# Kernel tuning notes

Hardware: AMD Instinct MI355X
Metric: run time of the kernel (lower is better)

Reference implementation:

```python
import jax, jax.numpy as jnp
import numpy as np

N = 100000   # nodes
F = 256      # input features
H = 128      # hidden_dim
E = 3200000  # edges
EPS = 1e-5   # LayerNorm eps (torch default)


def setup_inputs() -> dict:
    key = jax.random.key(0)
    ks = jax.random.split(key, 8)
    x = jax.random.normal(ks[0], (N, F), dtype=jnp.float32)
    edge_index = jax.random.randint(ks[1], (2, E), 0, N, dtype=jnp.int64)
    W1 = jax.random.normal(ks[2], (F, H), dtype=jnp.float32) * 0.05
    b1 = jnp.zeros((H,), jnp.float32)
    g1 = jnp.ones((H,), jnp.float32)
    be1 = jnp.zeros((H,), jnp.float32)
    W2 = jax.random.normal(ks[3], (H, H // 2), dtype=jnp.float32) * 0.05
    b2 = jnp.zeros((H // 2,), jnp.float32)
    g2 = jnp.ones((H // 2,), jnp.float32)
    be2 = jnp.zeros((H // 2,), jnp.float32)
    Wr = jax.random.normal(ks[4], (H // 2, 1), dtype=jnp.float32) * 0.05
    br = jnp.zeros((1,), jnp.float32)
    return {"x": x, "edge_index": edge_index, "W1": W1, "b1": b1, "g1": g1,
            "be1": be1, "W2": W2, "b2": b2, "g2": g2, "be2": be2,
            "Wr": Wr, "br": br}


def gcn_conv(x, src, dst, norm, W, b, n):
    # transform then propagate: out[dst] += norm_e * (x @ W)[src]
    h = x @ W                                   # [n, out]
    msg = h[src] * norm[:, None]                # [E+n, out] gather + scale
    out = jax.ops.segment_sum(msg, dst, num_segments=n)  # scatter-add
    return out + b


def layer_norm(x, g, b):
    mu = jnp.mean(x, axis=-1, keepdims=True)
    var = jnp.mean(jnp.square(x - mu), axis=-1, keepdims=True)
    return (x - mu) * jax.lax.rsqrt(var + EPS) * g + b


def reference(x, edge_index, W1, b1, g1, be1, W2, b2, g2, be2, Wr, br):
    n = x.shape[0]
    loop = jnp.arange(n, dtype=edge_index.dtype)
    src = jnp.concatenate([edge_index[0], loop])  # self-loops appended
    dst = jnp.concatenate([edge_index[1], loop])
    # symmetric normalization: deg includes self-loop, so deg >= 1
    deg = jax.ops.segment_sum(jnp.ones_like(src, dtype=x.dtype), dst, num_segments=n)
    dinv = jax.lax.rsqrt(deg)
    norm = dinv[src] * dinv[dst]                # [E+n]

    h = gcn_conv(x, src, dst, norm, W1, b1, n)
    h = jax.nn.relu(layer_norm(h, g1, be1))     # dropout is identity in eval
    h = gcn_conv(h, src, dst, norm, W2, b2, n)
    h = jax.nn.relu(layer_norm(h, g2, be2))
    out = jax.nn.sigmoid(h @ Wr + br)           # [N, 1]
    # torch .squeeze(0) is a no-op since N != 1
    return out
```

## Files before the change

### kernel.cpp

```cpp
#include <hip/hip_runtime.h>
#include <math.h>
#include <stdint.h>


#define DEG_CAP 96
#define MAXBUCKET 400
#define BSHIFT 8
#define SCAN_B 1024

typedef _Float16 half_t;
typedef __attribute__((ext_vector_type(2))) _Float16 half2v;
typedef __attribute__((ext_vector_type(8))) _Float16 half8;
typedef __attribute__((ext_vector_type(4))) float f32x4;
typedef __attribute__((ext_vector_type(2))) float f32x2;

__device__ __forceinline__ uint32_t pack2(float a, float b) {
    half2v h; h.x = (half_t)a; h.y = (half_t)b;
    return __builtin_bit_cast(uint32_t, h);
}
__device__ __forceinline__ float2 unpack2(uint32_t u) {
    half2v h = __builtin_bit_cast(half2v, u);
    return make_float2((float)h.x, (float)h.y);
}

__device__ __forceinline__ float wave_reduce_sum(float x) {
#pragma unroll
    for (int o = 32; o >= 1; o >>= 1) x += __shfl_xor(x, o, 64);
    return x;
}

__global__ void k_detect(const int* __restrict__ ei, int* __restrict__ flag,
                         uint32_t* __restrict__ h1s, uint32_t* __restrict__ h2s,
                         int N) {
    const int t = threadIdx.x;
    if (t == 0) {
        int all_zero = 1;
        for (int i = 1; i < 128; i += 2)
            if (ei[i] != 0) all_zero = 0;
        *flag = all_zero;
    }
    if (t < 32) h1s[(size_t)N * 32 + t] = 0;
    else if (t < 48) h2s[(size_t)N * 16 + (t - 32)] = 0;
}

__device__ __forceinline__ int load_idx(const int* __restrict__ ei,
                                        long long pos, int is64) {
    if (is64) return (int)((const long long*)ei)[pos];
    return ei[pos];
}

__global__ __launch_bounds__(256) void k_w1t(const float* __restrict__ W1,
                                             uint16_t* __restrict__ w1t) {
    int idx = blockIdx.x * 256 + threadIdx.x;
    int m = idx >> 8, k = idx & 255;
    half_t v = (half_t)W1[k * 128 + m];
    w1t[idx] = __builtin_bit_cast(uint16_t, v);
}

__global__ __launch_bounds__(256) void k_hist(
    const int* __restrict__ ei, const int* __restrict__ flag,
    int* __restrict__ blkcnt, long long E, int P, int nbucket, int chunk) {
    __shared__ int hist[MAXBUCKET];
    for (int j = threadIdx.x; j < nbucket; j += 256) hist[j] = 0;
    __syncthreads();
    const int is64 = *flag;
    long long c0 = (long long)blockIdx.x * chunk;
    long long c1 = c0 + chunk; if (c1 > E) c1 = E;
    for (long long e = c0 + threadIdx.x; e < c1; e += 256) {
        int d = load_idx(ei, E + e, is64);
        atomicAdd(&hist[d >> BSHIFT], 1);
    }
    __syncthreads();
    for (int j = threadIdx.x; j < nbucket; j += 256)
        blkcnt[j * P + blockIdx.x] = hist[j];
}

__global__ __launch_bounds__(SCAN_B) void k_scan_local(
    const int* __restrict__ in, int* __restrict__ pre,
    int* __restrict__ partials, int M) {
    __shared__ int sh[SCAN_B];
    int i = blockIdx.x * SCAN_B + threadIdx.x;
    int v = (i < M) ? in[i] : 0;
    sh[threadIdx.x] = v;
    __syncthreads();
    for (int o = 1; o < SCAN_B; o <<= 1) {
        int t = (threadIdx.x >= o) ? sh[threadIdx.x - o] : 0;
        __syncthreads();
        sh[threadIdx.x] += t;
        __syncthreads();
    }
    if (i < M) pre[i] = sh[threadIdx.x] - v;
    if (threadIdx.x == SCAN_B - 1) partials[blockIdx.x] = sh[SCAN_B - 1];
}

__global__ __launch_bounds__(1024) void k_scan_partials(
    const int* __restrict__ partials, int* __restrict__ pscan, int NB) {
    __shared__ int sh[1024];
    int v = (threadIdx.x < NB) ? partials[threadIdx.x] : 0;
    sh[threadIdx.x] = v;
    __syncthreads();
    for (int o = 1; o < 1024; o <<= 1) {
        int t = (threadIdx.x >= o) ? sh[threadIdx.x - o] : 0;
        __syncthreads();
        sh[threadIdx.x] += t;
        __syncthreads();
    }
    pscan[threadIdx.x] = sh[threadIdx.x] - v;
}

__global__ __launch_bounds__(SCAN_B) void k_scan_add(
    const int* __restrict__ pre, const int* __restrict__ pscan,
    int* __restrict__ boff, int M) {
    int i = blockIdx.x * SCAN_B + threadIdx.x;
    if (i < M) boff[i] = pre[i] + pscan[blockIdx.x];
}

__global__ __launch_bounds__(256) void k_scatter_gemm(
    const int* __restrict__ ei, const int* __restrict__ flag,
    const int* __restrict__ boff, int2* __restrict__ ebuf,
    const float* __restrict__ x, const uint16_t* __restrict__ w1t,
    uint32_t* __restrict__ h1w, int n_gemm, int P, int nbucket, int chunk,
    long long E, int N) {
    __shared__ uint32_t xhw[64 * 132];
    __shared__ int cur[MAXBUCKET];
    const int sub = blockIdx.x % 3, grp = blockIdx.x / 3;

    if (sub == 0) {
        if (grp >= P) return;
        const int is64 = *flag;
        for (int j = threadIdx.x; j < nbucket; j += 256)
            cur[j] = boff[j * P + grp];
        __syncthreads();
        long long c0 = (long long)grp * chunk;
        long long c1 = c0 + chunk; if (c1 > E) c1 = E;
        for (long long e = c0 + threadIdx.x; e < c1; e += 256) {
            int s = load_idx(ei, e, is64);
            int d = load_idx(ei, E + e, is64);
            int pos = atomicAdd(&cur[d >> BSHIFT], 1);
            ebuf[pos] = make_int2(s, d & ((1 << BSHIFT) - 1));
        }
        return;
    }

    const int gb = grp * 2 + (sub - 1);
    if (gb >= n_gemm) return;
    const int t = threadIdx.x;
    const int row0 = gb * 64;

#pragma unroll
    for (int i = 0; i < 16; ++i) {
        int idx = t + i * 256;
        int r = idx >> 6, c4 = idx & 63;
        int rg = row0 + r; if (rg >= N) rg = N - 1;
        float4 v = ((const float4*)(x + (long long)rg * 256))[c4];
        uint2 p;
        p.x = pack2(v.x, v.y);
        p.y = pack2(v.z, v.w);
        *(uint2*)&xhw[r * 132 + 2 * c4] = p;
    }
    __syncthreads();

    const int lane = t & 63, w = t >> 6;
    const int r = lane & 15, g = lane >> 4;
    const int node = row0 + 16 * w + r;

    f32x4 acc[8];
#pragma unroll
    for (int mt = 0; mt < 8; ++mt) acc[mt] = (f32x4)0.0f;

    const uint32_t* xrow = &xhw[(16 * w + r) * 132];
#pragma unroll
    for (int ks = 0; ks < 8; ++ks) {
        half8 bfr = *(const half8*)&xrow[16 * ks + 4 * g];
#pragma unroll
        for (int mt = 0; mt < 8; ++mt) {
            half8 afr = *(const half8*)(w1t + ((16 * mt + r) * 256 + 32 * ks + 8 * g));
            acc[mt] = __builtin_amdgcn_mfma_f32_16x16x32_f16(afr, bfr, acc[mt], 0, 0, 0);
        }
    }

    if (node < N) {
#pragma unroll
        for (int mt = 0; mt < 8; ++mt) {
            uint2 pv;
            pv.x = pack2(acc[mt][0], acc[mt][1]);
            pv.y = pack2(acc[mt][2], acc[mt][3]);
            *(uint2*)&h1w[(long long)node * 64 + 8 * mt + 2 * g] = pv;
        }
    }
}

__global__ __launch_bounds__(256) void k_rankplace(
    const int2* __restrict__ ebuf, const int* __restrict__ boff,
    int* __restrict__ csr, int* __restrict__ cnt, float* __restrict__ dinv,
    const uint32_t* __restrict__ h1, uint16_t* __restrict__ h1s,
    int P, int nbucket, int N, long long E) {
    __shared__ int c256[256];
    __shared__ float dl[256];
    const int k = blockIdx.x;
    c256[threadIdx.x] = 0;
    __syncthreads();
    const int beg = boff[k * P];
    const int end = (k + 1 < nbucket) ? boff[(k + 1) * P] : (int)E;
    for (int i = beg + threadIdx.x; i < end; i += 256) {
        int2 sd = ebuf[i];
        int r = atomicAdd(&c256[sd.y], 1);
        if (r < DEG_CAP) csr[((k << BSHIFT) + sd.y) * DEG_CAP + r] = sd.x;
    }
    __syncthreads();
    const int base_node = k << BSHIFT;
    const int node = base_node + threadIdx.x;
    float dv = rsqrtf((float)c256[threadIdx.x] + 1.0f);
    dl[threadIdx.x] = dv;
    if (node < N) {
        cnt[node] = c256[threadIdx.x];
        dinv[node] = dv;
        int cn = min(c256[threadIdx.x], DEG_CAP);
        int cnp = (cn + 15) & ~15;
        for (int r = cn; r < cnp; ++r) csr[node * DEG_CAP + r] = N;
    }
    __syncthreads();
    const int nloc = min(256, N - base_node);
    for (int i = threadIdx.x; i < nloc * 64; i += 256) {
        const int loc = i >> 6;
        const float dvl = dl[loc];
        const long long w = (long long)(base_node + loc) * 64 + (i & 63);
        float2 v = unpack2(h1[w]);
        int p = __builtin_amdgcn_cvt_pk_fp8_f32(v.x * dvl, v.y * dvl, 0, false);
        h1s[w] = (uint16_t)p;
    }
}

__global__ __launch_bounds__(512) void k_agg1(
    const int* __restrict__ cnt, const float* __restrict__ dinv,
    const int* __restrict__ csr, const uint8_t* __restrict__ h1s,
    const float* __restrict__ b, const float* __restrict__ g,
    const float* __restrict__ be, const float* __restrict__ W2,
    uint8_t* __restrict__ h2s, int N) {
    __shared__ float W2s[128 * 64];
    __shared__ float zs[8][132];
    const int t = threadIdx.x;

#pragma unroll
    for (int i = 0; i < 4; ++i) {
        int idx = t + i * 512;
        ((float4*)W2s)[idx] = ((const float4*)W2)[idx];
    }
    __syncthreads();

    const int lane = t & 63, wave = t >> 6;
    const int node = blockIdx.x * 8 + wave;
    if (node >= N) return;

    const float di = dinv[node];
    const int cn = min(cnt[node], DEG_CAP);
    const int cnp = (cn + 15) & ~15;
    const int base = node * DEG_CAP;
    const int loff = lane << 1;

    uint32_t us = *(const uint16_t*)(h1s + ((size_t)node << 7) + loff);
    f32x2 acc = __builtin_amdgcn_cvt_pk_f32_fp8(us, false);

    for (int e = 0; e < cnp; e += 16) {
        int idx[16];
        *(int4*)&idx[0]  = *(const int4*)&csr[base + e];
        *(int4*)&idx[4]  = *(const int4*)&csr[base + e + 4];
        *(int4*)&idx[8]  = *(const int4*)&csr[base + e + 8];
        *(int4*)&idx[12] = *(const int4*)&csr[base + e + 12];
        uint32_t u[16];
#pragma unroll
        for (int j = 0; j < 16; ++j)
            u[j] = *(const uint16_t*)(h1s + ((size_t)idx[j] << 7) + loff);
#pragma unroll
        for (int j = 0; j < 16; ++j) {
            f32x2 v = __builtin_amdgcn_cvt_pk_f32_fp8(u[j], false);
            acc += v;
        }
    }
    float a0 = acc.x * di, a1 = acc.y * di;

    float x0 = a0 + b[lane * 2], x1 = a1 + b[lane * 2 + 1];
    float mu = wave_reduce_sum(x0 + x1) * (1.0f / 128.0f);
    float d0 = x0 - mu, d1 = x1 - mu;
    float var = wave_reduce_sum(d0 * d0 + d1 * d1) * (1.0f / 128.0f);
    float rs = rsqrtf(var + 1e-5f);
    float o0 = fmaxf(fmaf(d0 * rs, g[lane * 2], be[lane * 2]), 0.0f);
    float o1 = fmaxf(fmaf(d1 * rs, g[lane * 2 + 1], be[lane * 2 + 1]), 0.0f);

    *(float2*)&zs[wave][lane * 2] = make_float2(o0, o1);

    float acc2 = 0.0f;
#pragma unroll
    for (int k = 0; k < 128; k += 4) {
        float4 zv = *(const float4*)&zs[wave][k];
        acc2 = fmaf(zv.x, W2s[(k + 0) * 64 + lane], acc2);
        acc2 = fmaf(zv.y, W2s[(k + 1) * 64 + lane], acc2);
        acc2 = fmaf(zv.z, W2s[(k + 2) * 64 + lane], acc2);
        acc2 = fmaf(zv.w, W2s[(k + 3) * 64 + lane], acc2);
    }
    int p = __builtin_amdgcn_cvt_pk_fp8_f32(acc2 * di, 0.0f, 0, false);
    h2s[((size_t)node << 6) + lane] = (uint8_t)p;
}

__global__ __launch_bounds__(256) void k_agg2(
    const int* __restrict__ cnt, const float* __restrict__ dinv,
    const int* __restrict__ csr, const uint8_t* __restrict__ h2s,
    const float* __restrict__ b2, const float* __restrict__ g2,
    const float* __restrict__ be2, const float* __restrict__ Wr,
    const float* __restrict__ br, float* __restrict__ out, int N) {
    const int lane = threadIdx.x & 63;
    const int node = blockIdx.x * 4 + (threadIdx.x >> 6);
    if (node >= N) return;
    const float di = dinv[node];
    const int cn = min(cnt[node], DEG_CAP);
    const int cnp = (cn + 15) & ~15;
    const int base = node * DEG_CAP;

    float a = __builtin_amdgcn_cvt_f32_fp8(h2s[((size_t)node << 6) + lane], 0);
    for (int e = 0; e < cnp; e += 16) {
        int idx[16];
        *(int4*)&idx[0]  = *(const int4*)&csr[base + e];
        *(int4*)&idx[4]  = *(const int4*)&csr[base + e + 4];
        *(int4*)&idx[8]  = *(const int4*)&csr[base + e + 8];
        *(int4*)&idx[12] = *(const int4*)&csr[base + e + 12];
        uint32_t u[16];
#pragma unroll
        for (int j = 0; j < 16; ++j)
            u[j] = h2s[((size_t)idx[j] << 6) + lane];
#pragma unroll
        for (int j = 0; j < 16; ++j)
            a += __builtin_amdgcn_cvt_f32_fp8(u[j], 0);
    }
    a *= di;

    float x = a + b2[lane];
    float mu = wave_reduce_sum(x) * (1.0f / 64.0f);
    float d = x - mu;
    float var = wave_reduce_sum(d * d) * (1.0f / 64.0f);
    float zz = fmaxf(fmaf(d * rsqrtf(var + 1e-5f), g2[lane], be2[lane]), 0.0f);
    float dot = wave_reduce_sum(zz * Wr[lane]);
    if (lane == 0) out[node] = 1.0f / (1.0f + expf(-(dot + br[0])));
}

extern "C" void kernel_launch(void* const* d_in, const int* in_sizes, int n_in,
                              void* d_out, int out_size, void* d_ws,
                              size_t ws_size, hipStream_t stream) {
    const float* x   = (const float*)d_in[0];
    const int*   ei  = (const int*)d_in[1];
    const float* W1  = (const float*)d_in[2];
    const float* b1  = (const float*)d_in[3];
    const float* g1  = (const float*)d_in[4];
    const float* be1 = (const float*)d_in[5];
    const float* W2  = (const float*)d_in[6];
    const float* b2  = (const float*)d_in[7];
    const float* g2  = (const float*)d_in[8];
    const float* be2 = (const float*)d_in[9];
    const float* Wr  = (const float*)d_in[10];
    const float* br  = (const float*)d_in[11];
    float* out = (float*)d_out;

    const int N = in_sizes[0] / 256;
    const long long E = in_sizes[1] / 2;

    const int nbucket = (N + 255) >> BSHIFT;
    const int NG = (N + 63) / 64;
    const int P = 782;
    const int chunk = (int)((E + P - 1) / P);
    const int M = nbucket * P;
    const int NB = (M + SCAN_B - 1) / SCAN_B;

    int* wsI = (int*)d_ws;
    size_t off = 0;
    int* flag    = wsI + off; off += 64;
    int* cnt     = wsI + off; off += (size_t)((N + 63) / 64) * 64;
    float* dinv  = (float*)(wsI + off); off += (size_t)((N + 63) / 64) * 64;
    int* blkcnt  = wsI + off; off += (size_t)((M + 63) / 64) * 64;
    int* pre     = wsI + off; off += (size_t)((M + 63) / 64) * 64;
    int* partials= wsI + off; off += 1024;
    int* pscan   = wsI + off; off += 1024;
    uint16_t* w1t= (uint16_t*)(wsI + off); off += 16384;
    int2* ebuf   = (int2*)(wsI + off); off += (size_t)(2 * E);
    int* csr     = wsI + off; off += (size_t)N * DEG_CAP;
    uint32_t* h1 = (uint32_t*)(wsI + off); off += (size_t)N * 64;
    uint32_t* h1s= (uint32_t*)(wsI + off); off += (size_t)(N + 1) * 32;
    uint32_t* h2s= (uint32_t*)(wsI + off); off += (size_t)(N + 1) * 16;

    k_detect<<<1, 64, 0, stream>>>(ei, flag, h1s, h2s, N);
    k_w1t<<<128, 256, 0, stream>>>(W1, w1t);

    k_hist<<<P, 256, 0, stream>>>(ei, flag, blkcnt, E, P, nbucket, chunk);
    k_scan_local<<<NB, SCAN_B, 0, stream>>>(blkcnt, pre, partials, M);
    k_scan_partials<<<1, 1024, 0, stream>>>(partials, pscan, NB);
    k_scan_add<<<NB, SCAN_B, 0, stream>>>(pre, pscan, blkcnt, M);

    k_scatter_gemm<<<3 * P, 256, 0, stream>>>(ei, flag, blkcnt, ebuf,
                                              x, w1t, h1, NG,
                                              P, nbucket, chunk, E, N);

    k_rankplace<<<nbucket, 256, 0, stream>>>(ebuf, blkcnt, csr, cnt, dinv,
                                             h1, (uint16_t*)h1s,
                                             P, nbucket, N, E);

    k_agg1<<<(N + 7) / 8, 512, 0, stream>>>(cnt, dinv, csr, (const uint8_t*)h1s,
                                            b1, g1, be1, W2, (uint8_t*)h2s, N);

    k_agg2<<<(N + 3) / 4, 256, 0, stream>>>(cnt, dinv, csr, (const uint8_t*)h2s,
                                            b2, g2, be2, Wr, br, out, N);
}
```

Before: 336.5 us.

## Pack edge buffer into 32-bit words and widen per-lane gathers in aggregation

The bucketed edge buffer now stores the source index and the 8-bit local destination in one 32-bit word instead of an int2, halving its write and read traffic between scatter and rank-place. Both aggregation kernels change their lane mapping so each lane loads 4 fp8 features (32-bit) per neighbor. Sub-groups of the wave then handle different neighbors in parallel and are combined with xor-shuffles, cutting the number of narrow gather instructions. The packing assumes node ids fit in 24 bits. The wave-level reductions are rescaled to account for the replicated lanes.

```diff
diff --git a/kernel.cpp b/kernel.cpp
--- a/kernel.cpp
+++ b/kernel.cpp
@@ -117,7 +117,7 @@
 
 __global__ __launch_bounds__(256) void k_scatter_gemm(
     const int* __restrict__ ei, const int* __restrict__ flag,
-    const int* __restrict__ boff, int2* __restrict__ ebuf,
+    const int* __restrict__ boff, int* __restrict__ ebuf,
     const float* __restrict__ x, const uint16_t* __restrict__ w1t,
     uint32_t* __restrict__ h1w, int n_gemm, int P, int nbucket, int chunk,
     long long E, int N) {
@@ -137,7 +137,7 @@
             int s = load_idx(ei, e, is64);
             int d = load_idx(ei, E + e, is64);
             int pos = atomicAdd(&cur[d >> BSHIFT], 1);
-            ebuf[pos] = make_int2(s, d & ((1 << BSHIFT) - 1));
+            ebuf[pos] = s | ((d & ((1 << BSHIFT) - 1)) << 24);
         }
         return;
     }
@@ -191,7 +191,7 @@
 }
 
 __global__ __launch_bounds__(256) void k_rankplace(
-    const int2* __restrict__ ebuf, const int* __restrict__ boff,
+    const int* __restrict__ ebuf, const int* __restrict__ boff,
     int* __restrict__ csr, int* __restrict__ cnt, float* __restrict__ dinv,
     const uint32_t* __restrict__ h1, uint16_t* __restrict__ h1s,
     int P, int nbucket, int N, long long E) {
@@ -203,9 +203,11 @@
     const int beg = boff[k * P];
     const int end = (k + 1 < nbucket) ? boff[(k + 1) * P] : (int)E;
     for (int i = beg + threadIdx.x; i < end; i += 256) {
-        int2 sd = ebuf[i];
-        int r = atomicAdd(&c256[sd.y], 1);
-        if (r < DEG_CAP) csr[((k << BSHIFT) + sd.y) * DEG_CAP + r] = sd.x;
+        int v = ebuf[i];
+        int s = v & 0x00FFFFFF;
+        int dl8 = (unsigned)v >> 24;
+        int r = atomicAdd(&c256[dl8], 1);
+        if (r < DEG_CAP) csr[((k << BSHIFT) + dl8) * DEG_CAP + r] = s;
     }
     __syncthreads();
     const int base_node = k << BSHIFT;
@@ -252,42 +254,78 @@
     const int node = blockIdx.x * 8 + wave;
     if (node >= N) return;
 
+    const int c = lane & 31, half = lane >> 5;
     const float di = dinv[node];
     const int cn = min(cnt[node], DEG_CAP);
     const int cnp = (cn + 15) & ~15;
     const int base = node * DEG_CAP;
-    const int loff = lane << 1;
-
-    uint32_t us = *(const uint16_t*)(h1s + ((size_t)node << 7) + loff);
-    f32x2 acc = __builtin_amdgcn_cvt_pk_f32_fp8(us, false);
+    const int coff = c << 2;
+
+    size_t selfrow = (half == 0) ? (size_t)node : (size_t)N;
+    uint32_t us = *(const uint32_t*)(h1s + (selfrow << 7) + coff);
+    f32x2 acc0 = __builtin_amdgcn_cvt_pk_f32_fp8(us, false);
+    f32x2 acc1 = __builtin_amdgcn_cvt_pk_f32_fp8(us, true);
 
     for (int e = 0; e < cnp; e += 16) {
-        int idx[16];
-        *(int4*)&idx[0]  = *(const int4*)&csr[base + e];
-        *(int4*)&idx[4]  = *(const int4*)&csr[base + e + 4];
-        *(int4*)&idx[8]  = *(const int4*)&csr[base + e + 8];
-        *(int4*)&idx[12] = *(const int4*)&csr[base + e + 12];
-        uint32_t u[16];
-#pragma unroll
-        for (int j = 0; j < 16; ++j)
-            u[j] = *(const uint16_t*)(h1s + ((size_t)idx[j] << 7) + loff);
-#pragma unroll
-        for (int j = 0; j < 16; ++j) {
-            f32x2 v = __builtin_amdgcn_cvt_pk_f32_fp8(u[j], false);
-            acc += v;
-        }
-    }
-    float a0 = acc.x * di, a1 = acc.y * di;
-
-    float x0 = a0 + b[lane * 2], x1 = a1 + b[lane * 2 + 1];
-    float mu = wave_reduce_sum(x0 + x1) * (1.0f / 128.0f);
-    float d0 = x0 - mu, d1 = x1 - mu;
-    float var = wave_reduce_sum(d0 * d0 + d1 * d1) * (1.0f / 128.0f);
+        int4 i0 = *(const int4*)&csr[base + e];
+        int4 i1 = *(const int4*)&csr[base + e + 4];
+        int4 i2 = *(const int4*)&csr[base + e + 8];
+        int4 i3 = *(const int4*)&csr[base + e + 12];
+        int s0 = half ? i0.y : i0.x;
+        int s1 = half ? i0.w : i0.z;
+        int s2 = half ? i1.y : i1.x;
+        int s3 = half ? i1.w : i1.z;
+        int s4 = half ? i2.y : i2.x;
+        int s5 = half ? i2.w : i2.z;
+        int s6 = half ? i3.y : i3.x;
+        int s7 = half ? i3.w : i3.z;
+        uint32_t u0 = *(const uint32_t*)(h1s + ((size_t)s0 << 7) + coff);
+        uint32_t u1 = *(const uint32_t*)(h1s + ((size_t)s1 << 7) + coff);
+        uint32_t u2 = *(const uint32_t*)(h1s + ((size_t)s2 << 7) + coff);
+        uint32_t u3 = *(const uint32_t*)(h1s + ((size_t)s3 << 7) + coff);
+        uint32_t u4 = *(const uint32_t*)(h1s + ((size_t)s4 << 7) + coff);
+        uint32_t u5 = *(const uint32_t*)(h1s + ((size_t)s5 << 7) + coff);
+        uint32_t u6 = *(const uint32_t*)(h1s + ((size_t)s6 << 7) + coff);
+        uint32_t u7 = *(const uint32_t*)(h1s + ((size_t)s7 << 7) + coff);
+        acc0 += __builtin_amdgcn_cvt_pk_f32_fp8(u0, false);
+        acc1 += __builtin_amdgcn_cvt_pk_f32_fp8(u0, true);
+        acc0 += __builtin_amdgcn_cvt_pk_f32_fp8(u1, false);
+        acc1 += __builtin_amdgcn_cvt_pk_f32_fp8(u1, true);
+        acc0 += __builtin_amdgcn_cvt_pk_f32_fp8(u2, false);
+        acc1 += __builtin_amdgcn_cvt_pk_f32_fp8(u2, true);
+        acc0 += __builtin_amdgcn_cvt_pk_f32_fp8(u3, false);
+        acc1 += __builtin_amdgcn_cvt_pk_f32_fp8(u3, true);
+        acc0 += __builtin_amdgcn_cvt_pk_f32_fp8(u4, false);
+        acc1 += __builtin_amdgcn_cvt_pk_f32_fp8(u4, true);
+        acc0 += __builtin_amdgcn_cvt_pk_f32_fp8(u5, false);
+        acc1 += __builtin_amdgcn_cvt_pk_f32_fp8(u5, true);
+        acc0 += __builtin_amdgcn_cvt_pk_f32_fp8(u6, false);
+        acc1 += __builtin_amdgcn_cvt_pk_f32_fp8(u6, true);
+        acc0 += __builtin_amdgcn_cvt_pk_f32_fp8(u7, false);
+        acc1 += __builtin_amdgcn_cvt_pk_f32_fp8(u7, true);
+    }
+    acc0.x += __shfl_xor(acc0.x, 32); acc0.y += __shfl_xor(acc0.y, 32);
+    acc1.x += __shfl_xor(acc1.x, 32); acc1.y += __shfl_xor(acc1.y, 32);
+
+    float a0 = acc0.x * di, a1 = acc0.y * di;
+    float a2 = acc1.x * di, a3 = acc1.y * di;
+
+    float4 bv = *(const float4*)(b + 4 * c);
+    float x0 = a0 + bv.x, x1 = a1 + bv.y, x2 = a2 + bv.z, x3 = a3 + bv.w;
+    float mu = wave_reduce_sum(x0 + x1 + x2 + x3) * (1.0f / 256.0f);
+    float d0 = x0 - mu, d1 = x1 - mu, d2 = x2 - mu, d3 = x3 - mu;
+    float var = wave_reduce_sum(d0 * d0 + d1 * d1 + d2 * d2 + d3 * d3) *
+                (1.0f / 256.0f);
     float rs = rsqrtf(var + 1e-5f);
-    float o0 = fmaxf(fmaf(d0 * rs, g[lane * 2], be[lane * 2]), 0.0f);
-    float o1 = fmaxf(fmaf(d1 * rs, g[lane * 2 + 1], be[lane * 2 + 1]), 0.0f);
-
-    *(float2*)&zs[wave][lane * 2] = make_float2(o0, o1);
+    float4 gv = *(const float4*)(g + 4 * c);
+    float4 bev = *(const float4*)(be + 4 * c);
+    float o0 = fmaxf(fmaf(d0 * rs, gv.x, bev.x), 0.0f);
+    float o1 = fmaxf(fmaf(d1 * rs, gv.y, bev.y), 0.0f);
+    float o2 = fmaxf(fmaf(d2 * rs, gv.z, bev.z), 0.0f);
+    float o3 = fmaxf(fmaf(d3 * rs, gv.w, bev.w), 0.0f);
+
+    if (half == 0)
+        *(float4*)&zs[wave][4 * c] = make_float4(o0, o1, o2, o3);
 
     float acc2 = 0.0f;
 #pragma unroll
@@ -311,34 +349,66 @@
     const int lane = threadIdx.x & 63;
     const int node = blockIdx.x * 4 + (threadIdx.x >> 6);
     if (node >= N) return;
+    const int c = lane & 15, q = lane >> 4;
     const float di = dinv[node];
     const int cn = min(cnt[node], DEG_CAP);
     const int cnp = (cn + 15) & ~15;
     const int base = node * DEG_CAP;
-
-    float a = __builtin_amdgcn_cvt_f32_fp8(h2s[((size_t)node << 6) + lane], 0);
+    const int coff = c << 2;
+
+    size_t selfrow = (q == 0) ? (size_t)node : (size_t)N;
+    uint32_t us = *(const uint32_t*)(h2s + (selfrow << 6) + coff);
+    f32x2 acc0 = __builtin_amdgcn_cvt_pk_f32_fp8(us, false);
+    f32x2 acc1 = __builtin_amdgcn_cvt_pk_f32_fp8(us, true);
+
     for (int e = 0; e < cnp; e += 16) {
-        int idx[16];
-        *(int4*)&idx[0]  = *(const int4*)&csr[base + e];
-        *(int4*)&idx[4]  = *(const int4*)&csr[base + e + 4];
-        *(int4*)&idx[8]  = *(const int4*)&csr[base + e + 8];
-        *(int4*)&idx[12] = *(const int4*)&csr[base + e + 12];
-        uint32_t u[16];
-#pragma unroll
-        for (int j = 0; j < 16; ++j)
-            u[j] = h2s[((size_t)idx[j] << 6) + lane];
-#pragma unroll
-        for (int j = 0; j < 16; ++j)
-            a += __builtin_amdgcn_cvt_f32_fp8(u[j], 0);
-    }
-    a *= di;
-
-    float x = a + b2[lane];
-    float mu = wave_reduce_sum(x) * (1.0f / 64.0f);
-    float d = x - mu;
-    float var = wave_reduce_sum(d * d) * (1.0f / 64.0f);
-    float zz = fmaxf(fmaf(d * rsqrtf(var + 1e-5f), g2[lane], be2[lane]), 0.0f);
-    float dot = wave_reduce_sum(zz * Wr[lane]);
+        int4 i0 = *(const int4*)&csr[base + e];
+        int4 i1 = *(const int4*)&csr[base + e + 4];
+        int4 i2 = *(const int4*)&csr[base + e + 8];
+        int4 i3 = *(const int4*)&csr[base + e + 12];
+        int s0 = (q == 0) ? i0.x : (q == 1) ? i0.y : (q == 2) ? i0.z : i0.w;
+        int s1 = (q == 0) ? i1.x : (q == 1) ? i1.y : (q == 2) ? i1.z : i1.w;
+        int s2 = (q == 0) ? i2.x : (q == 1) ? i2.y : (q == 2) ? i2.z : i2.w;
+        int s3 = (q == 0) ? i3.x : (q == 1) ? i3.y : (q == 2) ? i3.z : i3.w;
+        uint32_t u0 = *(const uint32_t*)(h2s + ((size_t)s0 << 6) + coff);
+        uint32_t u1 = *(const uint32_t*)(h2s + ((size_t)s1 << 6) + coff);
+        uint32_t u2 = *(const uint32_t*)(h2s + ((size_t)s2 << 6) + coff);
+        uint32_t u3 = *(const uint32_t*)(h2s + ((size_t)s3 << 6) + coff);
+        acc0 += __builtin_amdgcn_cvt_pk_f32_fp8(u0, false);
+        acc1 += __builtin_amdgcn_cvt_pk_f32_fp8(u0, true);
+        acc0 += __builtin_amdgcn_cvt_pk_f32_fp8(u1, false);
+        acc1 += __builtin_amdgcn_cvt_pk_f32_fp8(u1, true);
+        acc0 += __builtin_amdgcn_cvt_pk_f32_fp8(u2, false);
+        acc1 += __builtin_amdgcn_cvt_pk_f32_fp8(u2, true);
+        acc0 += __builtin_amdgcn_cvt_pk_f32_fp8(u3, false);
+        acc1 += __builtin_amdgcn_cvt_pk_f32_fp8(u3, true);
+    }
+#pragma unroll
+    for (int off = 16; off <= 32; off <<= 1) {
+        acc0.x += __shfl_xor(acc0.x, off); acc0.y += __shfl_xor(acc0.y, off);
+        acc1.x += __shfl_xor(acc1.x, off); acc1.y += __shfl_xor(acc1.y, off);
+    }
+
+    float a0 = acc0.x * di, a1 = acc0.y * di;
+    float a2 = acc1.x * di, a3 = acc1.y * di;
+
+    float4 bv = *(const float4*)(b2 + 4 * c);
+    float x0 = a0 + bv.x, x1 = a1 + bv.y, x2 = a2 + bv.z, x3 = a3 + bv.w;
+    float mu = wave_reduce_sum(x0 + x1 + x2 + x3) * (1.0f / 256.0f);
+    float d0 = x0 - mu, d1 = x1 - mu, d2 = x2 - mu, d3 = x3 - mu;
+    float var = wave_reduce_sum(d0 * d0 + d1 * d1 + d2 * d2 + d3 * d3) *
+                (1.0f / 256.0f);
+    float rs = rsqrtf(var + 1e-5f);
+    float4 gv = *(const float4*)(g2 + 4 * c);
+    float4 bev = *(const float4*)(be2 + 4 * c);
+    float z0 = fmaxf(fmaf(d0 * rs, gv.x, bev.x), 0.0f);
+    float z1 = fmaxf(fmaf(d1 * rs, gv.y, bev.y), 0.0f);
+    float z2 = fmaxf(fmaf(d2 * rs, gv.z, bev.z), 0.0f);
+    float z3 = fmaxf(fmaf(d3 * rs, gv.w, bev.w), 0.0f);
+
+    float4 wv = *(const float4*)(Wr + 4 * c);
+    float dot = wave_reduce_sum(z0 * wv.x + z1 * wv.y + z2 * wv.z + z3 * wv.w)
+                * 0.25f;
     if (lane == 0) out[node] = 1.0f / (1.0f + expf(-(dot + br[0])));
 }
 
@@ -379,7 +449,7 @@
     int* partials= wsI + off; off += 1024;
     int* pscan   = wsI + off; off += 1024;
     uint16_t* w1t= (uint16_t*)(wsI + off); off += 16384;
-    int2* ebuf   = (int2*)(wsI + off); off += (size_t)(2 * E);
+    int* ebuf    = wsI + off; off += (size_t)E;
     int* csr     = wsI + off; off += (size_t)N * DEG_CAP;
     uint32_t* h1 = (uint32_t*)(wsI + off); off += (size_t)N * 64;
     uint32_t* h1s= (uint32_t*)(wsI + off); off += (size_t)(N + 1) * 32;
```

Measured after the change: 331.9 us. Within noise of the previous version (-1.4%).
